# Optimization experiments

Measured on AMD Instinct MI355X. Metric: run time of the kernel, lower is better.

## Reference

```python
import jax, jax.numpy as jnp
import numpy as np

# model hyperparameters (from init_kwargs)
N_IN = 2048
NN = 512
BATCH = 64
DT, TAU_M, TAU_X = 0.05, 10.0, 2.0
ALPHA = 1.0 - DT / TAU_M   # membrane decay
BETA = 1.0 - DT / TAU_X    # lateral-trace decay
V_TH = 2.0


def _loo_idx(nn):
    # leave-one-out gather indices: idx[j, n] = j if j < n else j + 1
    j = np.arange(nn - 1)[:, None]
    n = np.arange(nn)[None, :]
    return jnp.asarray(j + (j >= n))  # (nn-1, nn) int


def setup_inputs() -> dict:
    key = jax.random.key(0)
    k1, k2, k3, k4 = jax.random.split(key, 4)
    x = jax.random.uniform(k1, (BATCH, N_IN, NN), dtype=jnp.float32)      # per-neuron external input
    v = jax.random.normal(k2, (BATCH, NN), dtype=jnp.float32)             # membrane state
    z = jnp.zeros((BATCH, NN), dtype=jnp.float32)                         # previous spikes
    z_out = jax.random.uniform(k3, (BATCH, NN), dtype=jnp.float32)        # lateral spike trace
    w = jax.random.normal(k4, (N_IN + NN - 1, NN), dtype=jnp.float32) / np.sqrt(N_IN)
    return {"x": x, "v": v, "z": z, "z_out": z_out, "w": w}


def reference(x, v, z, z_out, w):
    # update lateral trace: z_out = beta * z_out + z (z detached in original)
    z_out_new = BETA * z_out + z
    # leave-one-out lateral input: z_loo[b, j, n] = z_out_new[b, j + (j >= n)]
    idx = _loo_idx(NN)
    z_loo = z_out_new[:, idx]  # (B, NN-1, NN)
    # membrane drive: sum_k x_tot[b,k,n] * w[k,n], where x_tot = cat([x, z_loo], dim=1)
    drive = (jnp.einsum('bkn,kn->bn', x, w[:N_IN])
             + jnp.einsum('bjn,jn->bn', z_loo, w[N_IN:]))
    v_new = ALPHA * v + drive - V_TH * z
    # thresholding nonlinearity -> output spikes
    z_new = (v_new - V_TH > 0).astype(v.dtype)
    return v_new, z_new, z_out_new
```

## Files before the change

### kernel.cpp

```cpp
#include <hip/hip_runtime.h>

#define BATCH 64
#define N_IN  2048
#define NN    512
#define NCH   64
#define THREADS 1024
#define ALPHA 0.995f
#define BETA  0.975f
#define V_TH  2.0f

__global__ __launch_bounds__(THREADS, 8)
void fused_step(const float* __restrict__ x,
                const float* __restrict__ v,
                const float* __restrict__ z,
                const float* __restrict__ z_out,
                const float* __restrict__ w,
                float* __restrict__ out)
{
    const int b    = blockIdx.y;
    const int nb   = blockIdx.x * NCH;
    const int tid  = threadIdx.x;
    const int nl   = tid & 15;
    const int kk   = tid >> 4;
    const int wid  = tid >> 6;
    const int lane = tid & 63;

    __shared__ float  zlds[NN];
    __shared__ float4 wpart[16][16];
    __shared__ float4 d1s[16];
    __shared__ float  red2[THREADS];

    for (int i = tid; i < NN; i += THREADS)
        zlds[i] = BETA * z_out[b * NN + i] + z[b * NN + i];

    const float4* __restrict__ x4 = (const float4*)(x + (size_t)b * N_IN * NN + nb);
    const float4* __restrict__ w4 = (const float4*)(w + nb);
    const float4* xp = x4 + (size_t)kk * (NN / 4) + nl;
    const float4* wp = w4 + (size_t)kk * (NN / 4) + nl;
    const size_t kstride = (size_t)64 * (NN / 4);

    float4 acc = make_float4(0.f, 0.f, 0.f, 0.f);
#pragma unroll 2
    for (int i = 0; i < 8; ++i) {
        float4 xv[4], wvv[4];
#pragma unroll
        for (int u = 0; u < 4; ++u) xv[u]  = xp[u * kstride];
#pragma unroll
        for (int u = 0; u < 4; ++u) wvv[u] = wp[u * kstride];
#pragma unroll
        for (int u = 0; u < 4; ++u) {
            acc.x += xv[u].x * wvv[u].x;
            acc.y += xv[u].y * wvv[u].y;
            acc.z += xv[u].z * wvv[u].z;
            acc.w += xv[u].w * wvv[u].w;
        }
        xp += 4 * kstride;
        wp += 4 * kstride;
    }

#pragma unroll
    for (int off = 32; off >= 16; off >>= 1) {
        acc.x += __shfl_down(acc.x, off);
        acc.y += __shfl_down(acc.y, off);
        acc.z += __shfl_down(acc.z, off);
        acc.w += __shfl_down(acc.w, off);
    }
    if (lane < 16) wpart[wid][lane] = acc;
    __syncthreads();

    const int n_loc = tid & 63;
    const int n     = nb + n_loc;
    const int jg    = tid >> 6;
    float d2 = 0.f;
    for (int j = jg; j < NN - 1; j += 16)
        d2 += zlds[j + (j >= n)] * w[(size_t)(N_IN + j) * NN + n];
    red2[tid] = d2;

    if (tid < 16) {
        float4 s = wpart[0][tid];
#pragma unroll
        for (int ww = 1; ww < 16; ++ww) {
            const float4 o = wpart[ww][tid];
            s.x += o.x; s.y += o.y; s.z += o.z; s.w += o.w;
        }
        d1s[tid] = s;
    }
    __syncthreads();

    if (tid < 64) {
        const float d1 = ((const float*)d1s)[n_loc];
        float d2s = 0.f;
#pragma unroll
        for (int g = 0; g < 16; ++g) d2s += red2[n_loc + 64 * g];
        const float vv = v[b * NN + n];
        const float zz = z[b * NN + n];
        const float v_new = ALPHA * vv + d1 + d2s - V_TH * zz;
        out[b * NN + n]                  = v_new;
        out[BATCH * NN + b * NN + n]     = (v_new - V_TH > 0.f) ? 1.f : 0.f;
        out[2 * BATCH * NN + b * NN + n] = zlds[n];
    }
}

extern "C" void kernel_launch(void* const* d_in, const int* in_sizes, int n_in,
                              void* d_out, int out_size, void* d_ws, size_t ws_size,
                              hipStream_t stream) {
    (void)in_sizes; (void)n_in; (void)out_size; (void)d_ws; (void)ws_size;
    const float* x     = (const float*)d_in[0];
    const float* v     = (const float*)d_in[1];
    const float* z     = (const float*)d_in[2];
    const float* z_out = (const float*)d_in[3];
    const float* w     = (const float*)d_in[4];
    float* out = (float*)d_out;

    dim3 grid(NN / NCH, BATCH);
    fused_step<<<grid, THREADS, 0, stream>>>(x, v, z, z_out, w, out);
}
```

Before: 57.83 us.

## Share weight loads across four batches per block with narrower neuron tiles

Each block now handles 4 batch rows and 16 neurons instead of 1 batch row and 64 neurons. A single w float4 load is reused for four x rows, and the lateral term is computed for all four batches in the block. This reduces redundant weight traffic from global memory and L2. In exchange, x accesses become 64-byte segments per row, which hurts coalescing, and the serial lateral-loop work is spread differently across threads.

After: 100.1 us. +73.0%, slower.

```diff
diff --git a/kernel.cpp b/kernel.cpp
--- a/kernel.cpp
+++ b/kernel.cpp
@@ -3,7 +3,8 @@
 #define BATCH 64
 #define N_IN  2048
 #define NN    512
-#define NCH   64
+#define NCH   16
+#define G     4
 #define THREADS 1024
 #define ALPHA 0.995f
 #define BETA  0.975f
@@ -17,87 +18,107 @@
                 const float* __restrict__ w,
                 float* __restrict__ out)
 {
-    const int b    = blockIdx.y;
-    const int nb   = blockIdx.x * NCH;
+    const int nc   = blockIdx.x;
+    const int bq   = blockIdx.y;
+    const int b0   = bq * G;
+    const int nb   = nc * NCH;
     const int tid  = threadIdx.x;
-    const int nl   = tid & 15;
-    const int kk   = tid >> 4;
+    const int nl   = tid & 3;
+    const int kk   = tid >> 2;
     const int wid  = tid >> 6;
     const int lane = tid & 63;
 
-    __shared__ float  zlds[NN];
-    __shared__ float4 wpart[16][16];
-    __shared__ float4 d1s[16];
+    __shared__ float  zlds[G][NN];
+    __shared__ float4 wpart[16][G][4];
+    __shared__ float  d1s[G][NCH];
     __shared__ float  red2[THREADS];
 
-    for (int i = tid; i < NN; i += THREADS)
-        zlds[i] = BETA * z_out[b * NN + i] + z[b * NN + i];
+    for (int i = tid; i < G * NN; i += THREADS) {
+        const int g = i >> 9, idx = i & 511;
+        zlds[g][idx] = BETA * z_out[(b0 + g) * NN + idx] + z[(b0 + g) * NN + idx];
+    }
 
-    const float4* __restrict__ x4 = (const float4*)(x + (size_t)b * N_IN * NN + nb);
-    const float4* __restrict__ w4 = (const float4*)(w + nb);
-    const float4* xp = x4 + (size_t)kk * (NN / 4) + nl;
-    const float4* wp = w4 + (size_t)kk * (NN / 4) + nl;
-    const size_t kstride = (size_t)64 * (NN / 4);
+    const float4* __restrict__ x4 = (const float4*)x;
+    const float4* __restrict__ w4 = (const float4*)w;
+    const int c4 = (nb >> 2) + nl;
 
-    float4 acc = make_float4(0.f, 0.f, 0.f, 0.f);
+    float4 acc[G];
+#pragma unroll
+    for (int g = 0; g < G; ++g) acc[g] = make_float4(0.f, 0.f, 0.f, 0.f);
+
 #pragma unroll 2
     for (int i = 0; i < 8; ++i) {
-        float4 xv[4], wvv[4];
+        const size_t roff = (size_t)(kk + 256 * i) * 128 + c4;
+        float4 xv[G];
 #pragma unroll
-        for (int u = 0; u < 4; ++u) xv[u]  = xp[u * kstride];
+        for (int g = 0; g < G; ++g)
+            xv[g] = x4[(size_t)(b0 + g) * (N_IN * 128) + roff];
+        const float4 wv = w4[roff];
 #pragma unroll
-        for (int u = 0; u < 4; ++u) wvv[u] = wp[u * kstride];
-#pragma unroll
-        for (int u = 0; u < 4; ++u) {
-            acc.x += xv[u].x * wvv[u].x;
-            acc.y += xv[u].y * wvv[u].y;
-            acc.z += xv[u].z * wvv[u].z;
-            acc.w += xv[u].w * wvv[u].w;
+        for (int g = 0; g < G; ++g) {
+            acc[g].x += xv[g].x * wv.x;
+            acc[g].y += xv[g].y * wv.y;
+            acc[g].z += xv[g].z * wv.z;
+            acc[g].w += xv[g].w * wv.w;
         }
-        xp += 4 * kstride;
-        wp += 4 * kstride;
     }
 
 #pragma unroll
-    for (int off = 32; off >= 16; off >>= 1) {
-        acc.x += __shfl_down(acc.x, off);
-        acc.y += __shfl_down(acc.y, off);
-        acc.z += __shfl_down(acc.z, off);
-        acc.w += __shfl_down(acc.w, off);
+    for (int off = 32; off >= 4; off >>= 1) {
+#pragma unroll
+        for (int g = 0; g < G; ++g) {
+            acc[g].x += __shfl_down(acc[g].x, off);
+            acc[g].y += __shfl_down(acc[g].y, off);
+            acc[g].z += __shfl_down(acc[g].z, off);
+            acc[g].w += __shfl_down(acc[g].w, off);
+        }
     }
-    if (lane < 16) wpart[wid][lane] = acc;
+    if (lane < 4) {
+#pragma unroll
+        for (int g = 0; g < G; ++g) wpart[wid][g][lane] = acc[g];
+    }
     __syncthreads();
 
-    const int n_loc = tid & 63;
-    const int n     = nb + n_loc;
-    const int jg    = tid >> 6;
-    float d2 = 0.f;
-    for (int j = jg; j < NN - 1; j += 16)
-        d2 += zlds[j + (j >= n)] * w[(size_t)(N_IN + j) * NN + n];
-    red2[tid] = d2;
-
     if (tid < 16) {
-        float4 s = wpart[0][tid];
+        const int g = tid >> 2, c = tid & 3;
+        float4 s = wpart[0][g][c];
 #pragma unroll
         for (int ww = 1; ww < 16; ++ww) {
-            const float4 o = wpart[ww][tid];
+            const float4 o = wpart[ww][g][c];
             s.x += o.x; s.y += o.y; s.z += o.z; s.w += o.w;
         }
-        d1s[tid] = s;
+        d1s[g][c * 4 + 0] = s.x;
+        d1s[g][c * 4 + 1] = s.y;
+        d1s[g][c * 4 + 2] = s.z;
+        d1s[g][c * 4 + 3] = s.w;
+    }
+
+    {
+        const int g     = tid >> 8;
+        const int rem   = tid & 255;
+        const int jg    = rem >> 4;
+        const int n_loc = rem & 15;
+        const int n     = nb + n_loc;
+        float d2 = 0.f;
+        for (int j = jg; j < NN - 1; j += 16)
+            d2 += zlds[g][j + (j >= n)] * w[(size_t)(N_IN + j) * NN + n];
+        red2[tid] = d2;
     }
     __syncthreads();
 
     if (tid < 64) {
-        const float d1 = ((const float*)d1s)[n_loc];
+        const int g     = tid >> 4;
+        const int n_loc = tid & 15;
+        const int n     = nb + n_loc;
         float d2s = 0.f;
 #pragma unroll
-        for (int g = 0; g < 16; ++g) d2s += red2[n_loc + 64 * g];
-        const float vv = v[b * NN + n];
-        const float zz = z[b * NN + n];
-        const float v_new = ALPHA * vv + d1 + d2s - V_TH * zz;
-        out[b * NN + n]                  = v_new;
-        out[BATCH * NN + b * NN + n]     = (v_new - V_TH > 0.f) ? 1.f : 0.f;
-        out[2 * BATCH * NN + b * NN + n] = zlds[n];
+        for (int jg = 0; jg < 16; ++jg) d2s += red2[g * 256 + jg * 16 + n_loc];
+        const float vv    = v[(b0 + g) * NN + n];
+        const float zz    = z[(b0 + g) * NN + n];
+        const float v_new = ALPHA * vv + d1s[g][n_loc] + d2s - V_TH * zz;
+        out[(b0 + g) * NN + n]                  = v_new;
+        out[BATCH * NN + (b0 + g) * NN + n]     = (v_new - V_TH > 0.f) ? 1.f : 0.f;
+        out[2 * BATCH * NN + (b0 + g) * NN + n] = zlds[g][n];
     }
 }
 
@@ -112,6 +133,6 @@
     const float* w     = (const float*)d_in[4];
     float* out = (float*)d_out;
 
-    dim3 grid(NN / NCH, BATCH);
+    dim3 grid(NN / NCH, BATCH / G);
     fused_step<<<grid, THREADS, 0, stream>>>(x, v, z, z_out, w, out);
 }
```
